# Kernel optimization log

Measured on AMD Instinct MI355X. Metric: run time of the kernel, lower is better.

Reference implementation:

```python
import jax, jax.numpy as jnp
import numpy as np

B, K, S, E = 16, 16, 512, 512   # batch, k_history, max_spikes_in_batch, embed_dim
L, H, KVH, D = 16, 8, 2, 64     # num_latents, heads, kv heads, head_dim
BIN = 50                        # bin_size (RoPE table length)


def setup_inputs() -> dict:
    key = jax.random.key(0)
    ks = jax.random.split(key, 8)
    spike = jax.random.normal(ks[0], (B, K, S, E), dtype=jnp.float32)
    offsets = jax.random.randint(ks[1], (B, K, S), 0, BIN)
    spike_lengths = jax.random.randint(ks[2], (B, K), 1, S + 1)  # >=1 so no fully-masked row
    # standard RoPE tables of shape (BIN, D)
    inv_freq = 1.0 / (10000.0 ** (np.arange(0, D, 2, dtype=np.float32) / D))
    freqs = np.outer(np.arange(BIN, dtype=np.float32), inv_freq)      # (BIN, D/2)
    emb = np.concatenate([freqs, freqs], axis=-1)                     # (BIN, D)
    cos = jnp.asarray(np.cos(emb), dtype=jnp.float32)
    sin = jnp.asarray(np.sin(emb), dtype=jnp.float32)
    latent_query = jax.random.normal(ks[3], (L, E), dtype=jnp.float32)
    Wq = jax.random.normal(ks[4], (H * D, E), dtype=jnp.float32) * (E ** -0.5)
    Wk = jax.random.normal(ks[5], (KVH * D, E), dtype=jnp.float32) * (E ** -0.5)
    Wv = jax.random.normal(ks[6], (KVH * D, E), dtype=jnp.float32) * (E ** -0.5)
    Wo = jax.random.normal(ks[7], (E, H * D), dtype=jnp.float32) * ((H * D) ** -0.5)
    return dict(spike=spike, offsets=offsets, spike_lengths=spike_lengths,
                cos=cos, sin=sin, latent_query=latent_query,
                Wq=Wq, Wk=Wk, Wv=Wv, Wo=Wo)


def rotate_half(x):
    h = x.shape[-1] // 2
    return jnp.concatenate([-x[..., h:], x[..., :h]], axis=-1)


def reference(spike, offsets, spike_lengths, cos, sin, latent_query, Wq, Wk, Wv, Wo):
    n_rep = H // KVH
    # fixed learnable queries, shared across batch / k_history
    xq = (latent_query @ Wq.T).reshape(L, H, D)                         # (L,H,D)
    xk = jnp.einsum('bkse,he->bksh', spike, Wk).reshape(B, K, S, KVH, D)
    xv = jnp.einsum('bkse,he->bksh', spike, Wv).reshape(B, K, S, KVH, D)
    # inline RoPE on keys only (is_decoder=False), driven by per-token offsets
    cos_sel = cos[offsets][..., None, :]                                # (B,K,S,1,D)
    sin_sel = sin[offsets][..., None, :]
    xk = xk * cos_sel + rotate_half(xk) * sin_sel
    # repeat_kv: interleaved head repetition (matches torch expand+reshape)
    xk = jnp.repeat(xk, n_rep, axis=3)                                  # (B,K,S,H,D)
    xv = jnp.repeat(xv, n_rep, axis=3)
    scores = jnp.einsum('lhd,bkshd->bkhls', xq, xk) / jnp.sqrt(jnp.float32(D))
    # ragged-length mask: positions >= spike_lengths are invalid
    pos = jnp.arange(S)
    mask = pos[None, None, None, None, :] >= spike_lengths[:, :, None, None, None]
    scores = jnp.where(mask, -jnp.inf, scores)
    attn = jax.nn.softmax(scores, axis=-1)                              # (B,K,H,L,S)
    out = jnp.einsum('bkhls,bkshd->bklhd', attn, xv).reshape(B, K, L, H * D)
    return out @ Wo.T                                                   # (B,K,L,E)
```

## Files before the change

kernel.cpp:

```cpp
#include <hip/hip_runtime.h>
#include <hip/hip_bf16.h>
#include <stdint.h>

typedef __attribute__((ext_vector_type(8))) short bf16x8;
typedef __attribute__((ext_vector_type(4))) float f32x4;

union FragU { uint4 u; bf16x8 v; };

#define Bn 16
#define Kn 16
#define Sn 512
#define En 512
#define Ln 16
#define Hn 8
#define Dn 64
#define BKTOT 256
#define MTOT (BKTOT*Sn)

__device__ __forceinline__ uint32_t pack_bf16(float lo, float hi) {
  uint32_t a = __float_as_uint(lo) + 0x8000u;
  uint32_t b = __float_as_uint(hi) + 0x8000u;
  return __builtin_amdgcn_perm(b, a, 0x07060302u);
}
__device__ __forceinline__ uint16_t bf16_1(float x) {
  __hip_bfloat16 h = __float2bfloat16(x);
  return *(uint16_t*)&h;
}
__device__ __forceinline__ void gload_lds16(const void* g, void* l) {
  __builtin_amdgcn_global_load_lds(
      (const __attribute__((address_space(1))) uint32_t*)g,
      (__attribute__((address_space(3))) uint32_t*)l, 16, 0, 0);
}

__global__ __launch_bounds__(256)
void xq_kernel(const float* __restrict__ latent, const float* __restrict__ Wq,
               float* __restrict__ xq)
{
  const int j = blockIdx.x;
  const int t = threadIdx.x;
  const float w0 = Wq[j*En + t];
  const float w1 = Wq[j*En + t + 256];
  float part[Ln];
#pragma unroll
  for (int l = 0; l < Ln; ++l)
    part[l] = w0 * latent[l*En + t] + w1 * latent[l*En + t + 256];
#pragma unroll
  for (int l = 0; l < Ln; ++l) {
    float v = part[l];
#pragma unroll
    for (int off = 32; off > 0; off >>= 1) v += __shfl_down(v, off, 64);
    part[l] = v;
  }
  __shared__ float red[4][Ln];
  const int lane = t & 63, wv = t >> 6;
  if (lane == 0) {
#pragma unroll
    for (int l = 0; l < Ln; ++l) red[wv][l] = part[l];
  }
  __syncthreads();
  if (t < Ln)
    xq[t*En + j] = red[0][t] + red[1][t] + red[2][t] + red[3][t];
}

__global__ __launch_bounds__(256)
void wconv_kernel(const float* __restrict__ Wk, const float* __restrict__ Wv,
                  const float* __restrict__ Wo,
                  uint4* __restrict__ Wsw, uint4* __restrict__ Wob)
{
  const int t = threadIdx.x;
  const int b = blockIdx.x;
  if (b < 64) {
    const int idx = b*256 + t;
    const int kb = idx >> 11;
    const int rem = idx & 2047;
    const int n = rem >> 3, p = rem & 7;
    const int c = p ^ (n & 7);
    const float* src = (n < 128 ? Wk + (size_t)n*En : Wv + (size_t)(n-128)*En) + kb*64 + c*8;
    float4 v0 = *(const float4*)src;
    float4 v1 = *(const float4*)(src+4);
    uint4 o;
    o.x = pack_bf16(v0.x,v0.y); o.y = pack_bf16(v0.z,v0.w);
    o.z = pack_bf16(v1.x,v1.y); o.w = pack_bf16(v1.z,v1.w);
    Wsw[idx] = o;
  } else {
    const int idx = (b-64)*256 + t;
    const float* src = Wo + (size_t)idx*8;
    float4 v0 = *(const float4*)src;
    float4 v1 = *(const float4*)(src+4);
    uint4 o;
    o.x = pack_bf16(v0.x,v0.y); o.y = pack_bf16(v0.z,v0.w);
    o.z = pack_bf16(v1.x,v1.y); o.w = pack_bf16(v1.z,v1.w);
    Wob[idx] = o;
  }
}

__global__ __launch_bounds__(256)
void kvproj_kernel(const float* __restrict__ spike, const int* __restrict__ offsets,
                   const float* __restrict__ cosT, const float* __restrict__ sinT,
                   const uint4* __restrict__ Wsw, const int* __restrict__ lengths,
                   uint16_t* __restrict__ Kbuf, uint16_t* __restrict__ Vt)
{
  __shared__ __align__(16) uint16_t Bs[256*64];
  __shared__ __align__(16) uint16_t As[64*72];
  const int t = threadIdx.x;
  const int bk   = blockIdx.x >> 3;
  const int tile = blockIdx.x & 7;
  if (tile * 64 >= lengths[bk]) return;
  const int m0 = blockIdx.x * 64;
  const int lane = t & 63, wv = t >> 6;
  const int quad = lane >> 4, lr = lane & 15;

  f32x4 acc[4][4];
#pragma unroll
  for (int i=0;i<4;i++)
#pragma unroll
    for (int j=0;j<4;j++) acc[i][j] = (f32x4){0.f,0.f,0.f,0.f};

  const int arow = t >> 3;
  const int aseg = t & 7;

  for (int kb = 0; kb < 8; ++kb) {
    const char* gb = (const char*)(Wsw + kb*2048) + (wv*64 + lane)*16;
    char* lb = (char*)Bs + wv*1024;
#pragma unroll
    for (int i = 0; i < 8; ++i)
      gload_lds16(gb + i*4096, lb + i*4096);
#pragma unroll
    for (int j = 0; j < 2; ++j) {
      const int row = arow + 32*j;
      const float* src = &spike[(size_t)(m0+row)*En + kb*64 + aseg*8];
      float4 v0 = *(const float4*)src;
      float4 v1 = *(const float4*)(src+4);
      uint4 o;
      o.x = pack_bf16(v0.x,v0.y); o.y = pack_bf16(v0.z,v0.w);
      o.z = pack_bf16(v1.x,v1.y); o.w = pack_bf16(v1.z,v1.w);
      *(uint4*)&As[row*72 + aseg*8] = o;
    }
    __syncthreads();
#pragma unroll
    for (int kk = 0; kk < 2; ++kk) {
      const int c = kk*4 + quad;
      FragU aF[4], bF[4];
#pragma unroll
      for (int mi=0;mi<4;mi++) aF[mi].u = *(const uint4*)&As[(mi*16+lr)*72 + c*8];
#pragma unroll
      for (int ni=0;ni<4;ni++) {
        const int n = wv*64 + ni*16 + lr;
        bF[ni].u = *(const uint4*)&Bs[n*64 + (c ^ (n&7))*8];
      }
#pragma unroll
      for (int mi=0;mi<4;mi++)
#pragma unroll
        for (int ni=0;ni<4;ni++)
          acc[mi][ni] = __builtin_amdgcn_mfma_f32_16x16x32_bf16(aF[mi].v, bF[ni].v, acc[mi][ni], 0,0,0);
    }
    __syncthreads();
  }

  const int sbase = m0 & 511;
  if (wv < 2) {
#pragma unroll
    for (int mi=0;mi<4;mi++) {
#pragma unroll
      for (int r=0;r<4;r++) {
        const int s = sbase + mi*16 + quad*4 + r;
        const int off = offsets[m0 + mi*16 + quad*4 + r];
#pragma unroll
        for (int ni=0;ni<4;ni++) {
          const int d = ni*16 + lr;
          const float v = acc[mi][ni][r];
          const float p = acc[mi][ni^2][r];
          const float rot = (ni < 2) ? -p : p;
          const float cc  = cosT[off*Dn + d];
          const float sn  = sinT[off*Dn + d];
          Kbuf[((size_t)(bk*512 + s))*128 + wv*64 + d] = bf16_1(v*cc + rot*sn);
        }
      }
    }
  } else {
    const int nbase = (wv - 2) * 64;
#pragma unroll
    for (int mi=0;mi<4;mi++) {
#pragma unroll
      for (int ni=0;ni<4;ni++) {
        const int np = nbase + ni*16 + lr;
        const int s  = sbase + mi*16 + quad*4;
        uint2 pk;
        pk.x = pack_bf16(acc[mi][ni][0], acc[mi][ni][1]);
        pk.y = pack_bf16(acc[mi][ni][2], acc[mi][ni][3]);
        *(uint2*)&Vt[((size_t)(bk*128 + np))*512 + s] = pk;
      }
    }
  }
}

__global__ __launch_bounds__(256)
void attn_kernel(const float* __restrict__ xq, const uint16_t* __restrict__ Kbuf,
                 const uint16_t* __restrict__ Vt, const int* __restrict__ lengths,
                 uint16_t* __restrict__ attn_out)
{
  __shared__ __align__(16) uint16_t Ks [128*72];
  __shared__ __align__(16) uint16_t Vts[64*136];
  __shared__ __align__(16) uint16_t Ps [4*16*136];

  const int t = threadIdx.x;
  const int bk = blockIdx.x >> 1, kvh = blockIdx.x & 1;
  const int w = t >> 6, lane = t & 63;
  const int quad = lane >> 4, lr = lane & 15;
  const int h = kvh*4 + w;
  const int len = lengths[bk];

  FragU aQ[2];
#pragma unroll
  for (int kk=0;kk<2;kk++) {
    const float* qp = &xq[lr*En + h*Dn + kk*32 + quad*8];
    float4 q0 = *(const float4*)qp;
    float4 q1 = *(const float4*)(qp + 4);
    aQ[kk].u.x = pack_bf16(q0.x*0.125f, q0.y*0.125f);
    aQ[kk].u.y = pack_bf16(q0.z*0.125f, q0.w*0.125f);
    aQ[kk].u.z = pack_bf16(q1.x*0.125f, q1.y*0.125f);
    aQ[kk].u.w = pack_bf16(q1.z*0.125f, q1.w*0.125f);
  }

  float m_run[4], l_run[4], alpha[4];
  f32x4 oacc[4];
#pragma unroll
  for (int r=0;r<4;r++){ m_run[r] = -3.0e38f; l_run[r] = 0.f; }
#pragma unroll
  for (int nd=0;nd<4;nd++) oacc[nd] = (f32x4){0.f,0.f,0.f,0.f};

  const int krow = t >> 1, kseg = t & 1;
  const int vrow = t >> 2, vseg = t & 3;

  for (int c = 0; c < 4; ++c) {
    const int s0 = c * 128;
    if (s0 >= len) break;
    __syncthreads();
    {
      const uint16_t* g = &Kbuf[((size_t)(bk*512 + s0 + krow))*128 + kvh*64 + kseg*32];
      uint16_t* dst = &Ks[krow*72 + kseg*32];
      uint4 a0 = *(const uint4*)g, a1 = *(const uint4*)(g+8);
      uint4 a2 = *(const uint4*)(g+16), a3 = *(const uint4*)(g+24);
      *(uint4*)dst = a0; *(uint4*)(dst+8) = a1; *(uint4*)(dst+16) = a2; *(uint4*)(dst+24) = a3;

      const uint16_t* gv = &Vt[((size_t)(bk*128 + kvh*64 + vrow))*512 + s0 + vseg*32];
      uint16_t* dv = &Vts[vrow*136 + vseg*32];
      uint4 b0 = *(const uint4*)gv, b1 = *(const uint4*)(gv+8);
      uint4 b2 = *(const uint4*)(gv+16), b3 = *(const uint4*)(gv+24);
      *(uint4*)dv = b0; *(uint4*)(dv+8) = b1; *(uint4*)(dv+16) = b2; *(uint4*)(dv+24) = b3;
    }
    __syncthreads();

    f32x4 sc[8];
#pragma unroll
    for (int ni=0;ni<8;ni++) {
      FragU b0, b1;
      b0.u = *(const uint4*)&Ks[(ni*16+lr)*72 + quad*8];
      b1.u = *(const uint4*)&Ks[(ni*16+lr)*72 + 32 + quad*8];
      f32x4 a = (f32x4){0.f,0.f,0.f,0.f};
      a = __builtin_amdgcn_mfma_f32_16x16x32_bf16(aQ[0].v, b0.v, a, 0,0,0);
      a = __builtin_amdgcn_mfma_f32_16x16x32_bf16(aQ[1].v, b1.v, a, 0,0,0);
      sc[ni] = a;
    }
#pragma unroll
    for (int ni=0;ni<8;ni++)
      if (s0 + ni*16 + lr >= len)
        sc[ni] = (f32x4){-3.0e38f,-3.0e38f,-3.0e38f,-3.0e38f};

#pragma unroll
    for (int r=0;r<4;r++) {
      float mx = sc[0][r];
#pragma unroll
      for (int ni=1;ni<8;ni++) mx = fmaxf(mx, sc[ni][r]);
#pragma unroll
      for (int o=1;o<16;o<<=1) mx = fmaxf(mx, __shfl_xor(mx, o, 16));
      const float mnew = fmaxf(m_run[r], mx);
      alpha[r] = __expf(m_run[r] - mnew);
      m_run[r] = mnew;
      float ssum = 0.f;
#pragma unroll
      for (int ni=0;ni<8;ni++) {
        float p = __expf(sc[ni][r] - mnew);
        sc[ni][r] = p;
        ssum += p;
      }
#pragma unroll
      for (int o=1;o<16;o<<=1) ssum += __shfl_xor(ssum, o, 16);
      l_run[r] = l_run[r]*alpha[r] + ssum;
    }

#pragma unroll
    for (int ni=0;ni<8;ni++)
#pragma unroll
      for (int r=0;r<4;r++)
        Ps[(w*16 + quad*4 + r)*136 + ni*16 + lr] = bf16_1(sc[ni][r]);

#pragma unroll
    for (int nd=0;nd<4;nd++)
#pragma unroll
      for (int r=0;r<4;r++) oacc[nd][r] *= alpha[r];

#pragma unroll
    for (int kk=0;kk<4;kk++) {
      FragU aP;
      aP.u = *(const uint4*)&Ps[(w*16 + lr)*136 + kk*32 + quad*8];
#pragma unroll
      for (int nd=0;nd<4;nd++) {
        FragU bV;
        bV.u = *(const uint4*)&Vts[(nd*16+lr)*136 + kk*32 + quad*8];
        oacc[nd] = __builtin_amdgcn_mfma_f32_16x16x32_bf16(aP.v, bV.v, oacc[nd], 0,0,0);
      }
    }
  }

#pragma unroll
  for (int r=0;r<4;r++) {
    const float rs = 1.0f / l_run[r];
    const int l = quad*4 + r;
#pragma unroll
    for (int nd=0;nd<4;nd++)
      attn_out[((size_t)(bk*16 + l))*512 + h*64 + nd*16 + lr] = bf16_1(oacc[nd][r] * rs);
  }
}

__global__ __launch_bounds__(256)
void oproj_kernel(const uint16_t* __restrict__ Ab, const uint16_t* __restrict__ Wob,
                  float* __restrict__ out)
{
  __shared__ __align__(16) uint16_t As[128*72];
  __shared__ __align__(16) uint16_t Bs[128*72];
  const int t = threadIdx.x;
  const int m0 = (blockIdx.x >> 2) * 128;
  const int n0 = (blockIdx.x & 3) * 128;
  const int lane = t & 63, wv = t >> 6;
  const int quad = lane >> 4, lr = lane & 15;
  const int wm = wv >> 1, wn = wv & 1;

  f32x4 acc[4][4];
#pragma unroll
  for (int i=0;i<4;i++)
#pragma unroll
    for (int j=0;j<4;j++) acc[i][j] = (f32x4){0.f,0.f,0.f,0.f};

  const int srow = t >> 3, sseg = t & 7;
  for (int kb = 0; kb < 8; ++kb) {
#pragma unroll
    for (int j = 0; j < 4; ++j) {
      const int row = srow + 32*j;
      *(uint4*)&As[row*72 + sseg*8] = *(const uint4*)&Ab [(size_t)(m0+row)*512 + kb*64 + sseg*8];
      *(uint4*)&Bs[row*72 + sseg*8] = *(const uint4*)&Wob[(size_t)(n0+row)*512 + kb*64 + sseg*8];
    }
    __syncthreads();
#pragma unroll
    for (int kk = 0; kk < 2; ++kk) {
      const int c = kk*4 + quad;
      FragU aF[4], bF[4];
#pragma unroll
      for (int mi=0;mi<4;mi++) aF[mi].u = *(const uint4*)&As[(wm*64+mi*16+lr)*72 + c*8];
#pragma unroll
      for (int ni=0;ni<4;ni++) bF[ni].u = *(const uint4*)&Bs[(wn*64+ni*16+lr)*72 + c*8];
#pragma unroll
      for (int mi=0;mi<4;mi++)
#pragma unroll
        for (int ni=0;ni<4;ni++)
          acc[mi][ni] = __builtin_amdgcn_mfma_f32_16x16x32_bf16(aF[mi].v, bF[ni].v, acc[mi][ni], 0,0,0);
    }
    __syncthreads();
  }
#pragma unroll
  for (int mi=0;mi<4;mi++)
#pragma unroll
    for (int r=0;r<4;r++)
#pragma unroll
      for (int ni=0;ni<4;ni++)
        out[(size_t)(m0 + wm*64 + mi*16 + quad*4 + r)*512 + n0 + wn*64 + ni*16 + lr] = acc[mi][ni][r];
}

extern "C" void kernel_launch(void* const* d_in, const int* in_sizes, int n_in,
                              void* d_out, int out_size, void* d_ws, size_t ws_size,
                              hipStream_t stream)
{
  const float* spike   = (const float*)d_in[0];
  const int*   offsets = (const int*)d_in[1];
  const int*   lengths = (const int*)d_in[2];
  const float* cosT    = (const float*)d_in[3];
  const float* sinT    = (const float*)d_in[4];
  const float* latent  = (const float*)d_in[5];
  const float* Wq      = (const float*)d_in[6];
  const float* Wk      = (const float*)d_in[7];
  const float* Wv      = (const float*)d_in[8];
  const float* Wo      = (const float*)d_in[9];
  float* out = (float*)d_out;

  char* ws = (char*)d_ws;
  float*    xq   = (float*)ws;
  uint4*    Wsw  = (uint4*)(ws + 65536);
  uint4*    Wob  = (uint4*)(ws + 65536 + 262144);
  uint16_t* Kbuf = (uint16_t*)(ws + 1048576);
  uint16_t* Vt   = (uint16_t*)(ws + 1048576 + 33554432ull);
  uint16_t* attn_out = (uint16_t*)(ws + 1048576 + 67108864ull);

  hipLaunchKernelGGL(xq_kernel,     dim3(512),  dim3(256), 0, stream, latent, Wq, xq);
  hipLaunchKernelGGL(wconv_kernel,  dim3(192),  dim3(256), 0, stream, Wk, Wv, Wo, Wsw, Wob);
  hipLaunchKernelGGL(kvproj_kernel, dim3(2048), dim3(256), 0, stream, spike, offsets, cosT, sinT, Wsw, lengths, Kbuf, Vt);
  hipLaunchKernelGGL(attn_kernel,   dim3(512),  dim3(256), 0, stream, xq, Kbuf, Vt, lengths, attn_out);
  hipLaunchKernelGGL(oproj_kernel,  dim3(128),  dim3(256), 0, stream, attn_out, (const uint16_t*)Wob, out);
}
```

Before: 430.8 us.

## Split attention over sequence halves with merge kernel, fuse prep kernels, swizzle A tile

Merges the xq and weight-conversion kernels into one prep launch. Splits the attention kernel into two sequence halves per (bk, kv-head), doubling the grid, and adds a merge kernel that combines the partial outputs using their softmax max and sum statistics. The kvproj A tile drops its padding in favour of an XOR swizzle and gains a min-blocks occupancy hint. The cost is an extra launch and a float32 round trip for the partial outputs. The main time is kvproj, which is bound by reading spike, so the overall effect is likely small.

```diff
diff --git a/kernel.cpp b/kernel.cpp
--- a/kernel.cpp
+++ b/kernel.cpp
@@ -33,44 +33,39 @@
 }
 
 __global__ __launch_bounds__(256)
-void xq_kernel(const float* __restrict__ latent, const float* __restrict__ Wq,
-               float* __restrict__ xq)
-{
-  const int j = blockIdx.x;
-  const int t = threadIdx.x;
-  const float w0 = Wq[j*En + t];
-  const float w1 = Wq[j*En + t + 256];
-  float part[Ln];
-#pragma unroll
-  for (int l = 0; l < Ln; ++l)
-    part[l] = w0 * latent[l*En + t] + w1 * latent[l*En + t + 256];
-#pragma unroll
-  for (int l = 0; l < Ln; ++l) {
-    float v = part[l];
-#pragma unroll
-    for (int off = 32; off > 0; off >>= 1) v += __shfl_down(v, off, 64);
-    part[l] = v;
-  }
-  __shared__ float red[4][Ln];
-  const int lane = t & 63, wv = t >> 6;
-  if (lane == 0) {
-#pragma unroll
-    for (int l = 0; l < Ln; ++l) red[wv][l] = part[l];
-  }
-  __syncthreads();
-  if (t < Ln)
-    xq[t*En + j] = red[0][t] + red[1][t] + red[2][t] + red[3][t];
-}
-
-__global__ __launch_bounds__(256)
-void wconv_kernel(const float* __restrict__ Wk, const float* __restrict__ Wv,
-                  const float* __restrict__ Wo,
-                  uint4* __restrict__ Wsw, uint4* __restrict__ Wob)
+void prep_kernel(const float* __restrict__ latent, const float* __restrict__ Wq,
+                 const float* __restrict__ Wk, const float* __restrict__ Wv,
+                 const float* __restrict__ Wo,
+                 float* __restrict__ xq, uint4* __restrict__ Wsw, uint4* __restrict__ Wob)
 {
   const int t = threadIdx.x;
   const int b = blockIdx.x;
-  if (b < 64) {
-    const int idx = b*256 + t;
+  if (b < 512) {
+    const int j = b;
+    const float w0 = Wq[j*En + t];
+    const float w1 = Wq[j*En + t + 256];
+    float part[Ln];
+#pragma unroll
+    for (int l = 0; l < Ln; ++l)
+      part[l] = w0 * latent[l*En + t] + w1 * latent[l*En + t + 256];
+#pragma unroll
+    for (int l = 0; l < Ln; ++l) {
+      float v = part[l];
+#pragma unroll
+      for (int off = 32; off > 0; off >>= 1) v += __shfl_down(v, off, 64);
+      part[l] = v;
+    }
+    __shared__ float red[4][Ln];
+    const int lane = t & 63, wv = t >> 6;
+    if (lane == 0) {
+#pragma unroll
+      for (int l = 0; l < Ln; ++l) red[wv][l] = part[l];
+    }
+    __syncthreads();
+    if (t < Ln)
+      xq[t*En + j] = red[0][t] + red[1][t] + red[2][t] + red[3][t];
+  } else if (b < 576) {
+    const int idx = (b-512)*256 + t;
     const int kb = idx >> 11;
     const int rem = idx & 2047;
     const int n = rem >> 3, p = rem & 7;
@@ -83,7 +78,7 @@
     o.z = pack_bf16(v1.x,v1.y); o.w = pack_bf16(v1.z,v1.w);
     Wsw[idx] = o;
   } else {
-    const int idx = (b-64)*256 + t;
+    const int idx = (b-576)*256 + t;
     const float* src = Wo + (size_t)idx*8;
     float4 v0 = *(const float4*)src;
     float4 v1 = *(const float4*)(src+4);
@@ -94,14 +89,14 @@
   }
 }
 
-__global__ __launch_bounds__(256)
+__global__ __launch_bounds__(256, 4)
 void kvproj_kernel(const float* __restrict__ spike, const int* __restrict__ offsets,
                    const float* __restrict__ cosT, const float* __restrict__ sinT,
                    const uint4* __restrict__ Wsw, const int* __restrict__ lengths,
                    uint16_t* __restrict__ Kbuf, uint16_t* __restrict__ Vt)
 {
   __shared__ __align__(16) uint16_t Bs[256*64];
-  __shared__ __align__(16) uint16_t As[64*72];
+  __shared__ __align__(16) uint16_t As[64*64];
   const int t = threadIdx.x;
   const int bk   = blockIdx.x >> 3;
   const int tile = blockIdx.x & 7;
@@ -134,7 +129,7 @@
       uint4 o;
       o.x = pack_bf16(v0.x,v0.y); o.y = pack_bf16(v0.z,v0.w);
       o.z = pack_bf16(v1.x,v1.y); o.w = pack_bf16(v1.z,v1.w);
-      *(uint4*)&As[row*72 + aseg*8] = o;
+      *(uint4*)&As[row*64 + (aseg ^ (row & 7))*8] = o;
     }
     __syncthreads();
 #pragma unroll
@@ -142,7 +137,7 @@
       const int c = kk*4 + quad;
       FragU aF[4], bF[4];
 #pragma unroll
-      for (int mi=0;mi<4;mi++) aF[mi].u = *(const uint4*)&As[(mi*16+lr)*72 + c*8];
+      for (int mi=0;mi<4;mi++) aF[mi].u = *(const uint4*)&As[(mi*16+lr)*64 + (c ^ (lr & 7))*8];
 #pragma unroll
       for (int ni=0;ni<4;ni++) {
         const int n = wv*64 + ni*16 + lr;
@@ -197,18 +192,27 @@
 __global__ __launch_bounds__(256)
 void attn_kernel(const float* __restrict__ xq, const uint16_t* __restrict__ Kbuf,
                  const uint16_t* __restrict__ Vt, const int* __restrict__ lengths,
-                 uint16_t* __restrict__ attn_out)
+                 float* __restrict__ Opart, float* __restrict__ MLpart)
 {
   __shared__ __align__(16) uint16_t Ks [128*72];
   __shared__ __align__(16) uint16_t Vts[64*136];
   __shared__ __align__(16) uint16_t Ps [4*16*136];
 
   const int t = threadIdx.x;
-  const int bk = blockIdx.x >> 1, kvh = blockIdx.x & 1;
+  const int bk   = blockIdx.x >> 2;
+  const int kvh  = (blockIdx.x >> 1) & 1;
+  const int half = blockIdx.x & 1;
+  const int len = lengths[bk];
+  const size_t pbase = ((size_t)bk*2 + kvh)*2 + half;
+
+  if (half*256 >= len) {
+    if (t < 128) MLpart[pbase*128 + t] = (t & 1) ? 0.f : -3.0e38f;
+    return;
+  }
+
   const int w = t >> 6, lane = t & 63;
   const int quad = lane >> 4, lr = lane & 15;
   const int h = kvh*4 + w;
-  const int len = lengths[bk];
 
   FragU aQ[2];
 #pragma unroll
@@ -232,8 +236,8 @@
   const int krow = t >> 1, kseg = t & 1;
   const int vrow = t >> 2, vseg = t & 3;
 
-  for (int c = 0; c < 4; ++c) {
-    const int s0 = c * 128;
+  for (int ci = 0; ci < 2; ++ci) {
+    const int s0 = (half*2 + ci) * 128;
     if (s0 >= len) break;
     __syncthreads();
     {
@@ -315,11 +319,50 @@
 
 #pragma unroll
   for (int r=0;r<4;r++) {
-    const float rs = 1.0f / l_run[r];
     const int l = quad*4 + r;
+    const int hlL = w*16 + l;
 #pragma unroll
     for (int nd=0;nd<4;nd++)
-      attn_out[((size_t)(bk*16 + l))*512 + h*64 + nd*16 + lr] = bf16_1(oacc[nd][r] * rs);
+      Opart[pbase*4096 + hlL*64 + nd*16 + lr] = oacc[nd][r];
+    if (lr == 0) {
+      MLpart[pbase*128 + hlL*2]     = m_run[r];
+      MLpart[pbase*128 + hlL*2 + 1] = l_run[r];
+    }
+  }
+}
+
+__global__ __launch_bounds__(256)
+void attn_merge_kernel(const float* __restrict__ Opart, const float* __restrict__ MLpart,
+                       uint16_t* __restrict__ attn_out)
+{
+  const int bk = blockIdx.x;
+  const int t = threadIdx.x;
+  const int hlG = t >> 1;
+  const int dh = t & 1;
+  const int h = hlG >> 4;
+  const int l = hlG & 15;
+  const int kvh = h >> 2;
+  const int hlL = (h & 3)*16 + l;
+  const size_t pb = ((size_t)bk*2 + kvh)*2;
+
+  const float m1 = MLpart[pb*128 + hlL*2],       l1 = MLpart[pb*128 + hlL*2 + 1];
+  const float m2 = MLpart[(pb+1)*128 + hlL*2],   l2 = MLpart[(pb+1)*128 + hlL*2 + 1];
+  const float m  = fmaxf(m1, m2);
+  const float a1 = __expf(m1 - m), a2 = __expf(m2 - m);
+  const float inv = 1.0f / (a1*l1 + a2*l2);
+  const float w1 = a1*inv, w2 = a2*inv;
+
+  const float* O1 = &Opart[pb*4096 + hlL*64 + dh*32];
+  const float* O2 = &Opart[(pb+1)*4096 + hlL*64 + dh*32];
+  uint16_t* dst = &attn_out[((size_t)bk*16 + l)*512 + h*64 + dh*32];
+#pragma unroll
+  for (int i = 0; i < 8; ++i) {
+    float4 o1 = *(const float4*)(O1 + i*4);
+    float4 o2 = *(const float4*)(O2 + i*4);
+    uint2 pk;
+    pk.x = pack_bf16(w1*o1.x + w2*o2.x, w1*o1.y + w2*o2.y);
+    pk.y = pack_bf16(w1*o1.z + w2*o2.z, w1*o1.w + w2*o2.w);
+    *(uint2*)(dst + i*4) = pk;
   }
 }
 
@@ -397,12 +440,19 @@
   uint4*    Wsw  = (uint4*)(ws + 65536);
   uint4*    Wob  = (uint4*)(ws + 65536 + 262144);
   uint16_t* Kbuf = (uint16_t*)(ws + 1048576);
-  uint16_t* Vt   = (uint16_t*)(ws + 1048576 + 33554432ull);
-  uint16_t* attn_out = (uint16_t*)(ws + 1048576 + 67108864ull);
-
-  hipLaunchKernelGGL(xq_kernel,     dim3(512),  dim3(256), 0, stream, latent, Wq, xq);
-  hipLaunchKernelGGL(wconv_kernel,  dim3(192),  dim3(256), 0, stream, Wk, Wv, Wo, Wsw, Wob);
-  hipLaunchKernelGGL(kvproj_kernel, dim3(2048), dim3(256), 0, stream, spike, offsets, cosT, sinT, Wsw, lengths, Kbuf, Vt);
-  hipLaunchKernelGGL(attn_kernel,   dim3(512),  dim3(256), 0, stream, xq, Kbuf, Vt, lengths, attn_out);
-  hipLaunchKernelGGL(oproj_kernel,  dim3(128),  dim3(256), 0, stream, attn_out, (const uint16_t*)Wob, out);
-}
+  uint16_t* Vt   = (uint16_t*)(ws + 34603008ull);
+  uint16_t* attn_out = (uint16_t*)(ws + 68157440ull);
+  float*    Opart  = (float*)(ws + 72351744ull);
+  float*    MLpart = (float*)(ws + 89128960ull);
+
+  hipLaunchKernelGGL(prep_kernel,   dim3(704),  dim3(256), 0, stream,
+                     latent, Wq, Wk, Wv, Wo, xq, Wsw, Wob);
+  hipLaunchKernelGGL(kvproj_kernel, dim3(2048), dim3(256), 0, stream,
+                     spike, offsets, cosT, sinT, Wsw, lengths, Kbuf, Vt);
+  hipLaunchKernelGGL(attn_kernel,   dim3(1024), dim3(256), 0, stream,
+                     xq, Kbuf, Vt, lengths, Opart, MLpart);
+  hipLaunchKernelGGL(attn_merge_kernel, dim3(256), dim3(256), 0, stream,
+                     Opart, MLpart, attn_out);
+  hipLaunchKernelGGL(oproj_kernel,  dim3(128),  dim3(256), 0, stream,
+                     attn_out, (const uint16_t*)Wob, out);
+}
```

Measured after the change: 438.5 us. About the same (+1.8%).
